# Performance work log

Hardware: AMD Instinct MI355X
Metric: run time of the kernel (lower is better)

## Reference

```python
import jax, jax.numpy as jnp
import numpy as np
import math

IN_DIM = 3
N_LEVELS = 16
N_FEATS = 2
LOG2_HASHMAP = 19
BASE_RES = 16
DESIRED_RES = 2048
N_POINTS = 1048576
# first in_dim hash primes from the torch module; all fit in uint32
PRIMES = np.array([1, 2654435761, 805459861], dtype=np.uint32)


def _level_params():
    # faithful to the torch code: growth exponent divides by (base_resolution - 1)
    beta = math.exp((math.log(DESIRED_RES) - math.log(BASE_RES)) / (BASE_RES - 1))
    res = [math.floor(BASE_RES * beta ** i) for i in range(N_LEVELS)]
    hms = [min(r ** IN_DIM, 2 ** LOG2_HASHMAP) for r in res]
    return res, hms


def setup_inputs() -> dict:
    key = jax.random.key(0)
    kx, kt = jax.random.split(key)
    x = jax.random.uniform(kx, (N_POINTS, IN_DIM), dtype=jnp.float32)
    # kaiming_uniform(a=sqrt(5)) on [hashmap, n_feats] -> bound = sqrt(1/2)
    bound = math.sqrt(0.5)
    tables = jax.random.uniform(kt, (N_LEVELS, 2 ** LOG2_HASHMAP, N_FEATS),
                                dtype=jnp.float32, minval=-bound, maxval=bound)
    return {"x": x, "tables": tables}


def _forward(x, tables):
    res, hms = _level_params()
    neighbors = np.arange(1 << IN_DIM, dtype=np.int64).reshape(-1, 1)   # [8,1]
    dims = np.arange(IN_DIM, dtype=np.int64).reshape(1, -1)             # [1,3]
    bin_mask = jnp.asarray((neighbors & (1 << dims)) == 0)              # [8,3] bool
    primes = jnp.asarray(PRIMES)                                        # [3] uint32
    outs = [x]  # include_input=True
    for l in range(N_LEVELS):
        xs = x * jnp.float32(res[l])                    # [N,3]
        xi = jnp.floor(xs).astype(jnp.int32)            # torch .long() trunc; x>=0 so floor==trunc
        xf = xs - xi.astype(xs.dtype)                   # fractional part (no grad via xi)
        xi = xi[..., None, :]                           # [N,1,3]
        xf = xf[..., None, :]                           # [N,1,3]
        idx = jnp.where(bin_mask, xi, xi + 1).astype(jnp.uint32)         # [N,8,3]
        w = jnp.prod(jnp.where(bin_mask, 1.0 - xf, xf), axis=-1, keepdims=True)  # [N,8,1]
        # hash: (idx * prime) mod 2^32 (uint32 wraparound == int64 mul & 0xFFFFFFFF), xor-fold, mod size
        h = idx * primes                                # [N,8,3] uint32
        h = h[..., 0] ^ h[..., 1] ^ h[..., 2]           # [N,8]
        h = (h % jnp.uint32(hms[l])).astype(jnp.int32)
        emb = tables[l][h]                              # [N,8,F] gather
        outs.append(jnp.sum(emb * w, axis=-2))          # [N,F]
    return jnp.concatenate(outs, axis=-1)               # [N, 3 + 16*2]


def reference(x, tables):
    return _forward(x, tables)
```

## Files before the change

### kernel.cpp

```cpp
#include <hip/hip_runtime.h>
#include <math.h>
#include <stdint.h>

#define NPTS   1048576
#define NLEV   16
#define TPB    256
#define PPT    8
#define CHUNK  (TPB * PPT)
#define ROW    35
#define TBL_ENTRIES (1u << 19)

typedef float f4 __attribute__((ext_vector_type(4)));
typedef float f2 __attribute__((ext_vector_type(2)));

struct LevelParams {
    float    resf;
    uint32_t hm;
    uint32_t is_pow2;
    uint32_t pad;
    uint64_t magic;
};
struct LPAll { LevelParams lv[NLEV]; };

__device__ __forceinline__ void hash_calc(
    float xv0, float xv1, float xv2, const LevelParams& P,
    unsigned (&hi)[8], float (&w)[8])
{
    const float xs0 = xv0 * P.resf, xs1 = xv1 * P.resf, xs2 = xv2 * P.resf;
    const float f0 = floorf(xs0), f1 = floorf(xs1), f2v = floorf(xs2);
    const float t0 = xs0 - f0, t1 = xs1 - f1, t2 = xs2 - f2v;

    const unsigned a0 = (unsigned)(int)f0;
    const unsigned a1 = a0 + 1u;
    const unsigned b0 = (unsigned)(int)f1 * 2654435761u;
    const unsigned b1 = ((unsigned)(int)f1 + 1u) * 2654435761u;
    const unsigned c0 = (unsigned)(int)f2v * 805459861u;
    const unsigned c1 = ((unsigned)(int)f2v + 1u) * 805459861u;

    const float wa0 = 1.f - t0, wa1 = t0;
    const float wb0 = 1.f - t1, wb1 = t1;
    const float wc0 = 1.f - t2, wc1 = t2;

    const uint32_t hmv  = P.hm;
    const uint32_t mask = hmv - 1u;
    const uint64_t M    = P.magic;
    const bool     p2   = (P.is_pow2 != 0);

    #pragma unroll
    for (int n = 0; n < 8; ++n) {
        unsigned h = ((n & 1) ? a1 : a0)
                   ^ ((n & 2) ? b1 : b0)
                   ^ ((n & 4) ? c1 : c0);
        if (p2) {
            hi[n] = h & mask;
        } else {
            uint64_t low = M * (uint64_t)h;
            hi[n] = (uint32_t)(((__uint128_t)low * hmv) >> 64);
        }
        w[n] = (((n & 1) ? wa1 : wa0) * ((n & 2) ? wb1 : wb0))
               * ((n & 4) ? wc1 : wc0);
    }
}

__global__ __launch_bounds__(TPB)
void hashgrid_gather(const float* __restrict__ x,
                     const float* __restrict__ tables,
                     float* __restrict__ ws,
                     LPAll lp, int base)
{
    const int tid = threadIdx.x;
    const int lvl = base + (blockIdx.x & 7);
    const int p0  = (blockIdx.x >> 3) * CHUNK;

    const LevelParams P   = lp.lv[lvl];
    const f2*         tbl = (const f2*)(tables + (size_t)lvl * TBL_ENTRIES * 2);
    const float*      xp  = x + (size_t)p0 * 3;
    f2* wrow = (f2*)ws + (size_t)lvl * NPTS + p0;

    #pragma unroll
    for (int kk = 0; kk < PPT; kk += 2) {
        const int piA = tid + kk * TPB;
        const int piB = piA + TPB;

        const float xa0 = __builtin_nontemporal_load(&xp[piA * 3 + 0]);
        const float xa1 = __builtin_nontemporal_load(&xp[piA * 3 + 1]);
        const float xa2 = __builtin_nontemporal_load(&xp[piA * 3 + 2]);
        const float xb0 = __builtin_nontemporal_load(&xp[piB * 3 + 0]);
        const float xb1 = __builtin_nontemporal_load(&xp[piB * 3 + 1]);
        const float xb2 = __builtin_nontemporal_load(&xp[piB * 3 + 2]);

        unsigned hA[8]; float wA[8];
        unsigned hB[8]; float wB[8];
        hash_calc(xa0, xa1, xa2, P, hA, wA);
        hash_calc(xb0, xb1, xb2, P, hB, wB);

        f2 eA[8], eB[8];
        #pragma unroll
        for (int n = 0; n < 8; ++n) eA[n] = tbl[hA[n]];
        #pragma unroll
        for (int n = 0; n < 8; ++n) eB[n] = tbl[hB[n]];

        float accA0 = 0.f, accA1 = 0.f, accB0 = 0.f, accB1 = 0.f;
        #pragma unroll
        for (int n = 0; n < 8; ++n) {
            accA0 = fmaf(eA[n].x, wA[n], accA0);
            accA1 = fmaf(eA[n].y, wA[n], accA1);
        }
        #pragma unroll
        for (int n = 0; n < 8; ++n) {
            accB0 = fmaf(eB[n].x, wB[n], accB0);
            accB1 = fmaf(eB[n].y, wB[n], accB1);
        }

        f2 vA; vA.x = accA0; vA.y = accA1;
        f2 vB; vB.x = accB0; vB.y = accB1;
        __builtin_nontemporal_store(vA, &wrow[piA]);
        __builtin_nontemporal_store(vB, &wrow[piB]);
    }
}

__global__ __launch_bounds__(TPB)
void hashgrid_interleave(const float* __restrict__ x,
                         const float* __restrict__ ws,
                         float* __restrict__ out)
{
    __shared__ float srow[TPB * ROW];
    const int tid = threadIdx.x;
    const int p0  = blockIdx.x * TPB;

    const float* xblk = x + (size_t)p0 * 3;
    #pragma unroll
    for (int j = 0; j < 3; ++j) {
        int idx = tid + j * TPB;
        int p = idx / 3, c = idx - p * 3;
        srow[p * ROW + c] = __builtin_nontemporal_load(&xblk[idx]);
    }
    const f2* wsv = (const f2*)ws;
    #pragma unroll
    for (int l = 0; l < NLEV; ++l) {
        f2 v = __builtin_nontemporal_load(&wsv[(size_t)l * NPTS + p0 + tid]);
        srow[tid * ROW + 3 + 2 * l] = v.x;
        srow[tid * ROW + 4 + 2 * l] = v.y;
    }
    __syncthreads();

    f4*       outv = (f4*)(out + (size_t)p0 * ROW);
    const f4* sv   = (const f4*)srow;
    for (int j = tid; j < (TPB * ROW) / 4; j += TPB)
        __builtin_nontemporal_store(sv[j], &outv[j]);
}

__global__ __launch_bounds__(TPB)
void hashgrid_lvl(const float* __restrict__ x,
                  const float* __restrict__ tables,
                  float* __restrict__ out,
                  LPAll lp, int base)
{
    const int tid = threadIdx.x;
    const int lvl = base + (blockIdx.x & 7);
    const int p0  = (blockIdx.x >> 3) * TPB;

    const float* xp = x + (size_t)p0 * 3;
    const float xv0 = xp[tid * 3 + 0];
    const float xv1 = xp[tid * 3 + 1];
    const float xv2 = xp[tid * 3 + 2];

    const LevelParams P   = lp.lv[lvl];
    const f2*         tbl = (const f2*)(tables + (size_t)lvl * TBL_ENTRIES * 2);

    unsigned hi[8]; float w[8];
    hash_calc(xv0, xv1, xv2, P, hi, w);
    float acc0 = 0.f, acc1 = 0.f;
    #pragma unroll
    for (int n = 0; n < 8; ++n) {
        f2 e = tbl[hi[n]];
        acc0 = fmaf(e.x, w[n], acc0);
        acc1 = fmaf(e.y, w[n], acc1);
    }

    float* orow = out + (size_t)(p0 + tid) * ROW;
    __builtin_nontemporal_store(acc0, &orow[3 + 2 * lvl]);
    __builtin_nontemporal_store(acc1, &orow[4 + 2 * lvl]);
    if (lvl == 0) {
        __builtin_nontemporal_store(xv0, &orow[0]);
        __builtin_nontemporal_store(xv1, &orow[1]);
        __builtin_nontemporal_store(xv2, &orow[2]);
    }
}

extern "C" void kernel_launch(void* const* d_in, const int* in_sizes, int n_in,
                              void* d_out, int out_size, void* d_ws, size_t ws_size,
                              hipStream_t stream)
{
    const float* x      = (const float*)d_in[0];
    const float* tables = (const float*)d_in[1];
    float*       out    = (float*)d_out;

    LPAll lp;
    const double beta = exp((log(2048.0) - log(16.0)) / 15.0);
    for (int i = 0; i < NLEV; ++i) {
        double r = floor(16.0 * pow(beta, (double)i));
        double h3 = r * r * r;
        uint32_t hm = (h3 < (double)(1u << 19)) ? (uint32_t)h3 : (1u << 19);
        lp.lv[i].resf    = (float)r;
        lp.lv[i].hm      = hm;
        lp.lv[i].is_pow2 = ((hm & (hm - 1u)) == 0u) ? 1u : 0u;
        lp.lv[i].pad     = 0;
        lp.lv[i].magic   = lp.lv[i].is_pow2 ? 0ull : (~0ull / hm + 1ull);
    }

    const size_t ws_need = (size_t)NLEV * NPTS * 2 * sizeof(float);
    if (ws_size >= ws_need) {
        const int gblocks = 8 * (NPTS / CHUNK);
        hashgrid_gather<<<gblocks, TPB, 0, stream>>>(x, tables, (float*)d_ws, lp, 0);
        hashgrid_gather<<<gblocks, TPB, 0, stream>>>(x, tables, (float*)d_ws, lp, 8);
        hashgrid_interleave<<<NPTS / TPB, TPB, 0, stream>>>(x, (const float*)d_ws, out);
    } else {
        const int nblocks = 8 * (NPTS / TPB);
        hashgrid_lvl<<<nblocks, TPB, 0, stream>>>(x, tables, out, lp, 0);
        hashgrid_lvl<<<nblocks, TPB, 0, stream>>>(x, tables, out, lp, 8);
    }
}
```

Measured before the change: 476.3 us.

## Launch one gather kernel per level to keep each hash table cache-resident

The gather stage now launches 16 separate kernels, one per level, instead of two launches that each interleave 8 levels across blocks. Each launch reads only one 4 MB table, so its random lookups should stay within L2/MALL rather than competing with seven other tables. Per-thread work drops from 8 points to 2, which means more blocks per launch. The cost is 14 extra kernel launches and the x coordinates being read 16 times.

```diff
diff --git a/kernel.cpp b/kernel.cpp
--- a/kernel.cpp
+++ b/kernel.cpp
@@ -5,8 +5,6 @@
 #define NPTS   1048576
 #define NLEV   16
 #define TPB    256
-#define PPT    8
-#define CHUNK  (TPB * PPT)
 #define ROW    35
 #define TBL_ENTRIES (1u << 19)
 
@@ -63,60 +61,55 @@
 }
 
 __global__ __launch_bounds__(TPB)
-void hashgrid_gather(const float* __restrict__ x,
-                     const float* __restrict__ tables,
-                     float* __restrict__ ws,
-                     LPAll lp, int base)
+void hashgrid_gather1(const float* __restrict__ xall,
+                      const float* __restrict__ tb,
+                      f2* __restrict__ wrow_all,
+                      LevelParams P)
 {
     const int tid = threadIdx.x;
-    const int lvl = base + (blockIdx.x & 7);
-    const int p0  = (blockIdx.x >> 3) * CHUNK;
-
-    const LevelParams P   = lp.lv[lvl];
-    const f2*         tbl = (const f2*)(tables + (size_t)lvl * TBL_ENTRIES * 2);
-    const float*      xp  = x + (size_t)p0 * 3;
-    f2* wrow = (f2*)ws + (size_t)lvl * NPTS + p0;
-
-    #pragma unroll
-    for (int kk = 0; kk < PPT; kk += 2) {
-        const int piA = tid + kk * TPB;
-        const int piB = piA + TPB;
-
-        const float xa0 = __builtin_nontemporal_load(&xp[piA * 3 + 0]);
-        const float xa1 = __builtin_nontemporal_load(&xp[piA * 3 + 1]);
-        const float xa2 = __builtin_nontemporal_load(&xp[piA * 3 + 2]);
-        const float xb0 = __builtin_nontemporal_load(&xp[piB * 3 + 0]);
-        const float xb1 = __builtin_nontemporal_load(&xp[piB * 3 + 1]);
-        const float xb2 = __builtin_nontemporal_load(&xp[piB * 3 + 2]);
-
-        unsigned hA[8]; float wA[8];
-        unsigned hB[8]; float wB[8];
-        hash_calc(xa0, xa1, xa2, P, hA, wA);
-        hash_calc(xb0, xb1, xb2, P, hB, wB);
-
-        f2 eA[8], eB[8];
-        #pragma unroll
-        for (int n = 0; n < 8; ++n) eA[n] = tbl[hA[n]];
-        #pragma unroll
-        for (int n = 0; n < 8; ++n) eB[n] = tbl[hB[n]];
-
-        float accA0 = 0.f, accA1 = 0.f, accB0 = 0.f, accB1 = 0.f;
-        #pragma unroll
-        for (int n = 0; n < 8; ++n) {
-            accA0 = fmaf(eA[n].x, wA[n], accA0);
-            accA1 = fmaf(eA[n].y, wA[n], accA1);
-        }
-        #pragma unroll
-        for (int n = 0; n < 8; ++n) {
-            accB0 = fmaf(eB[n].x, wB[n], accB0);
-            accB1 = fmaf(eB[n].y, wB[n], accB1);
-        }
-
-        f2 vA; vA.x = accA0; vA.y = accA1;
-        f2 vB; vB.x = accB0; vB.y = accB1;
-        __builtin_nontemporal_store(vA, &wrow[piA]);
-        __builtin_nontemporal_store(vB, &wrow[piB]);
-    }
+    const int p0  = blockIdx.x * (TPB * 2);
+
+    const f2*    tbl = (const f2*)tb;
+    const float* xp  = xall + (size_t)p0 * 3;
+    f2*          wrow = wrow_all + p0;
+
+    const int piA = tid;
+    const int piB = tid + TPB;
+
+    const float xa0 = __builtin_nontemporal_load(&xp[piA * 3 + 0]);
+    const float xa1 = __builtin_nontemporal_load(&xp[piA * 3 + 1]);
+    const float xa2 = __builtin_nontemporal_load(&xp[piA * 3 + 2]);
+    const float xb0 = __builtin_nontemporal_load(&xp[piB * 3 + 0]);
+    const float xb1 = __builtin_nontemporal_load(&xp[piB * 3 + 1]);
+    const float xb2 = __builtin_nontemporal_load(&xp[piB * 3 + 2]);
+
+    unsigned hA[8]; float wA[8];
+    unsigned hB[8]; float wB[8];
+    hash_calc(xa0, xa1, xa2, P, hA, wA);
+    hash_calc(xb0, xb1, xb2, P, hB, wB);
+
+    f2 eA[8], eB[8];
+    #pragma unroll
+    for (int n = 0; n < 8; ++n) eA[n] = tbl[hA[n]];
+    #pragma unroll
+    for (int n = 0; n < 8; ++n) eB[n] = tbl[hB[n]];
+
+    float accA0 = 0.f, accA1 = 0.f, accB0 = 0.f, accB1 = 0.f;
+    #pragma unroll
+    for (int n = 0; n < 8; ++n) {
+        accA0 = fmaf(eA[n].x, wA[n], accA0);
+        accA1 = fmaf(eA[n].y, wA[n], accA1);
+    }
+    #pragma unroll
+    for (int n = 0; n < 8; ++n) {
+        accB0 = fmaf(eB[n].x, wB[n], accB0);
+        accB1 = fmaf(eB[n].y, wB[n], accB1);
+    }
+
+    f2 vA; vA.x = accA0; vA.y = accA1;
+    f2 vB; vB.x = accB0; vB.y = accB1;
+    __builtin_nontemporal_store(vA, &wrow[piA]);
+    __builtin_nontemporal_store(vB, &wrow[piB]);
 }
 
 __global__ __launch_bounds__(TPB)
@@ -211,9 +204,14 @@
 
     const size_t ws_need = (size_t)NLEV * NPTS * 2 * sizeof(float);
     if (ws_size >= ws_need) {
-        const int gblocks = 8 * (NPTS / CHUNK);
-        hashgrid_gather<<<gblocks, TPB, 0, stream>>>(x, tables, (float*)d_ws, lp, 0);
-        hashgrid_gather<<<gblocks, TPB, 0, stream>>>(x, tables, (float*)d_ws, lp, 8);
+        const int gblocks = NPTS / (TPB * 2);
+        for (int l = 0; l < NLEV; ++l) {
+            hashgrid_gather1<<<gblocks, TPB, 0, stream>>>(
+                x,
+                tables + (size_t)l * TBL_ENTRIES * 2,
+                (f2*)d_ws + (size_t)l * NPTS,
+                lp.lv[l]);
+        }
         hashgrid_interleave<<<NPTS / TPB, TPB, 0, stream>>>(x, (const float*)d_ws, out);
     } else {
         const int nblocks = 8 * (NPTS / TPB);
```

Measured after the change: 438.6 us. 1.09x faster.
